# Kernel optimization log

Measured on AMD Instinct MI355X. Metric: run time of the kernel, lower is better.

The kernel has to match this reference:

```python
import jax, jax.numpy as jnp
import numpy as np

N, E, F, H, L = 100000, 800000, 128, 128, 64


def _glorot(key, shape):
    lim = float(np.sqrt(6.0 / (shape[0] + shape[1])))
    return jax.random.uniform(key, shape, jnp.float32, -lim, lim)


def setup_inputs() -> dict:
    key = jax.random.key(0)
    ks = jax.random.split(key, 10)
    x = jax.random.normal(ks[0], (N, F), jnp.float32)
    noise = jax.random.normal(ks[1], (N, F), jnp.float32)
    edge_index = jax.random.randint(ks[2], (2, E), 0, N, jnp.int32)
    return {
        "x": x,
        "noise": noise,
        "edge_index": edge_index,
        "bn_gamma": jnp.ones((F,), jnp.float32),
        "bn_beta": jnp.zeros((F,), jnp.float32),
        "W1": _glorot(ks[3], (F, H)),
        "b1": jnp.zeros((H,), jnp.float32),
        "W2": _glorot(ks[4], (H + 2 * F, H)),
        "b2": jnp.zeros((H,), jnp.float32),
        "Wm": _glorot(ks[5], (H + F, L)),
        "bm": jnp.zeros((L,), jnp.float32),
        "Ws": _glorot(ks[6], (H + F, L)),
        "bs": jnp.zeros((L,), jnp.float32),
    }


def _gcn_conv(x, W, b, src, dst, norm, n):
    # GCNConv: transform, then sym-normalized sparse aggregation, then bias
    h = x @ W                                 # [n, out]
    msg = h[src] * norm[:, None]              # gather + scale  [E', out]
    return jax.ops.segment_sum(msg, dst, num_segments=n) + b


def reference(x, noise, edge_index, bn_gamma, bn_beta, W1, b1, W2, b2, Wm, bm, Ws, bs):
    n = x.shape[0]
    loops = jnp.arange(n, dtype=edge_index.dtype)
    src = jnp.concatenate([edge_index[0], loops])  # add self-loops
    dst = jnp.concatenate([edge_index[1], loops])
    deg = jax.ops.segment_sum(jnp.ones_like(src, dtype=x.dtype), dst, num_segments=n)
    dinv = jnp.where(deg > 0, jax.lax.rsqrt(jnp.maximum(deg, 1e-12)), 0.0)
    norm = dinv[src] * dinv[dst]                   # D^-1/2 A D^-1/2 edge weights

    # bn1 (training-mode batch norm over nodes)
    mu = x.mean(axis=0)
    var = x.var(axis=0)
    xb = (x - mu) * jax.lax.rsqrt(var + 1e-5) * bn_gamma + bn_beta

    h1 = jax.nn.relu(_gcn_conv(xb, W1, b1, src, dst, norm, n))
    h1 = jnp.concatenate([xb, noise, h1], axis=1)  # [n, H + 2F]
    h2 = jax.nn.relu(_gcn_conv(h1, W2, b2, src, dst, norm, n))
    # dropout(p=0.4) in eval mode -> identity
    last = jnp.concatenate([xb, h2], axis=1)       # [n, F + H]
    z_mean = _gcn_conv(last, Wm, bm, src, dst, norm, n)
    z_logstd = _gcn_conv(last, Ws, bs, src, dst, norm, n)
    return (z_mean, z_logstd)
```

## Files before the change

### kernel.cpp

```cpp
#include <hip/hip_runtime.h>
#include <math.h>


typedef short bf16x8 __attribute__((ext_vector_type(8)));
typedef float f32x4 __attribute__((ext_vector_type(4)));
typedef float f32x2 __attribute__((ext_vector_type(2)));

#define BN_G 1024
#define SCAN_BLK 256
#define SCAN_ELEMS 1024

__device__ inline unsigned short f2bf(float f) {
    unsigned int u = __builtin_bit_cast(unsigned int, f);
    u += 0x7fff + ((u >> 16) & 1);
    return (unsigned short)(u >> 16);
}
__device__ inline float bfl(unsigned int u) { return __builtin_bit_cast(float, u << 16); }
__device__ inline float bfh(unsigned int u) { return __builtin_bit_cast(float, u & 0xffff0000u); }
__device__ inline unsigned int pack2(float lo, float hi) {
    return ((unsigned int)f2bf(hi) << 16) | f2bf(lo);
}
__device__ inline f32x2 unp(unsigned int u) {
    return (f32x2){__builtin_bit_cast(float, u << 16),
                   __builtin_bit_cast(float, u & 0xffff0000u)};
}
__device__ inline void acc8v(f32x2* a, uint4 v) {
    a[0] += unp(v.x); a[1] += unp(v.y); a[2] += unp(v.z); a[3] += unp(v.w);
}

__device__ __forceinline__ void gload_lds16(const void* g, void* l) {
    __builtin_amdgcn_global_load_lds(
        (const __attribute__((address_space(1))) unsigned int*)g,
        (__attribute__((address_space(3))) unsigned int*)l, 16, 0, 0);
}

__global__ __launch_bounds__(256) void fused1(const float4* __restrict__ x4,
                                              float* __restrict__ partials, int n,
                                              const int* __restrict__ ei,
                                              int* __restrict__ cnt,
                                              int* __restrict__ slot, int E) {
    __shared__ float4 lds[2][8][32];
    int bid = blockIdx.x, t = threadIdx.x;
    if (bid < BN_G) {
        int cg = t & 31;
        int rs = t >> 5;
        float4 s = make_float4(0.f, 0.f, 0.f, 0.f);
        float4 q = make_float4(0.f, 0.f, 0.f, 0.f);
        const float4 z4 = make_float4(0.f, 0.f, 0.f, 0.f);
        const int stride = BN_G * 32;
        for (int r0 = bid * 32 + rs * 4; r0 < n; r0 += stride) {
            float4 v0 = x4[(size_t)r0 * 32 + cg];
            float4 v1 = (r0 + 1 < n) ? x4[(size_t)(r0 + 1) * 32 + cg] : z4;
            float4 v2 = (r0 + 2 < n) ? x4[(size_t)(r0 + 2) * 32 + cg] : z4;
            float4 v3 = (r0 + 3 < n) ? x4[(size_t)(r0 + 3) * 32 + cg] : z4;
            s.x += v0.x + v1.x + v2.x + v3.x;
            s.y += v0.y + v1.y + v2.y + v3.y;
            s.z += v0.z + v1.z + v2.z + v3.z;
            s.w += v0.w + v1.w + v2.w + v3.w;
            q.x = fmaf(v0.x, v0.x, fmaf(v1.x, v1.x, fmaf(v2.x, v2.x, fmaf(v3.x, v3.x, q.x))));
            q.y = fmaf(v0.y, v0.y, fmaf(v1.y, v1.y, fmaf(v2.y, v2.y, fmaf(v3.y, v3.y, q.y))));
            q.z = fmaf(v0.z, v0.z, fmaf(v1.z, v1.z, fmaf(v2.z, v2.z, fmaf(v3.z, v3.z, q.z))));
            q.w = fmaf(v0.w, v0.w, fmaf(v1.w, v1.w, fmaf(v2.w, v2.w, fmaf(v3.w, v3.w, q.w))));
        }
        lds[0][rs][cg] = s;
        lds[1][rs][cg] = q;
        __syncthreads();
        if (t < 64) {
            int which = t >> 5;
            int c = t & 31;
            float4 a = lds[which][0][c];
#pragma unroll
            for (int i = 1; i < 8; i++) {
                float4 b = lds[which][i][c];
                a.x += b.x; a.y += b.y; a.z += b.z; a.w += b.w;
            }
            int base = which * 128 + c * 4;
            partials[(size_t)(base + 0) * BN_G + bid] = a.x;
            partials[(size_t)(base + 1) * BN_G + bid] = a.y;
            partials[(size_t)(base + 2) * BN_G + bid] = a.z;
            partials[(size_t)(base + 3) * BN_G + bid] = a.w;
        }
    } else {
        int e = (bid - BN_G) * 256 + t;
        if (e < E) slot[e] = atomicAdd(&cnt[ei[E + e]], 1);
    }
}

__global__ __launch_bounds__(256) void fused2(const float4* __restrict__ partials4,
                                              float* __restrict__ stats,
                                              const int* __restrict__ cnt,
                                              int* __restrict__ row_ptr,
                                              int* __restrict__ bsums, int n) {
    __shared__ float red[256];
    __shared__ int lds[SCAN_BLK];
    int t = threadIdx.x;
    if (blockIdx.x < 256) {
        int c = blockIdx.x;
        float4 v = partials4[(size_t)c * (BN_G / 4) + t];
        red[t] = v.x + v.y + v.z + v.w;
        __syncthreads();
        for (int off = 128; off > 0; off >>= 1) {
            if (t < off) red[t] += red[t + off];
            __syncthreads();
        }
        if (t == 0) stats[c] = red[0];
    } else {
        int blk = blockIdx.x - 256;
        int base = blk * SCAN_ELEMS;
        int v[4];
        int s = 0;
#pragma unroll
        for (int j = 0; j < 4; j++) {
            int i = base + t * 4 + j;
            v[j] = s;
            s += (i < n) ? cnt[i] : 0;
        }
        lds[t] = s;
        __syncthreads();
        for (int off = 1; off < SCAN_BLK; off <<= 1) {
            int val = (t >= off) ? lds[t - off] : 0;
            __syncthreads();
            lds[t] += val;
            __syncthreads();
        }
        int excl = (t == 0) ? 0 : lds[t - 1];
#pragma unroll
        for (int j = 0; j < 4; j++) {
            int i = base + t * 4 + j;
            if (i < n) row_ptr[i] = excl + v[j];
        }
        if (t == SCAN_BLK - 1) bsums[blk] = lds[t];
    }
}

__global__ void fused3(int* __restrict__ bsums, int nb,
                       const float* __restrict__ stats,
                       const float* __restrict__ gamma, const float* __restrict__ beta,
                       float* __restrict__ scale, float* __restrict__ shift, float invN) {
    int t = threadIdx.x;
    if (t == 0) {
        int acc = 0;
        for (int i = 0; i < nb; i++) { int c = bsums[i]; bsums[i] = acc; acc += c; }
    } else if (t >= 128 && t < 256) {
        int c = t - 128;
        float mu = stats[c] * invN;
        float var = stats[128 + c] * invN - mu * mu;
        float sc = gamma[c] / sqrtf(var + 1e-5f);
        scale[c] = sc;
        shift[c] = beta[c] - mu * sc;
    }
}

__global__ void fused4(int* __restrict__ row_ptr, const int* __restrict__ bsums,
                       const int* __restrict__ cnt, float* __restrict__ dinv,
                       int n, int E) {
    int i = blockIdx.x * blockDim.x + threadIdx.x;
    if (i < n) {
        row_ptr[i] += bsums[i / SCAN_ELEMS];
        dinv[i] = rsqrtf((float)cnt[i] + 1.0f);
    }
    if (i == 0) row_ptr[n] = E;
}

__device__ inline void pack_body(int i, const float* __restrict__ W,
                                 unsigned short* __restrict__ Wp,
                                 int K, int C, int colOff) {
    if (i >= K * C) return;
    int k = i / C, c = i % C;
    int gc = c + colOff;
    int s = k >> 7, kc = (k >> 5) & 3, lhi = (k >> 3) & 3, j = k & 7;
    int wc = gc >> 6, n = (gc >> 4) & 3, l15 = gc & 15;
    int lane = lhi * 16 + l15;
    size_t dst = ((size_t)((s * 2 + wc) * 4 + kc) * 4 + n) * 512 + lane * 8 + j;
    Wp[dst] = f2bf(W[i]);
}

__global__ __launch_bounds__(256) void fused5(
    const int* __restrict__ ei, const int* __restrict__ row_ptr,
    const int* __restrict__ slot, int* __restrict__ edge_src, int E, int EB,
    const float4* __restrict__ x4, const float4* __restrict__ n4,
    const float* __restrict__ scale, const float* __restrict__ shift,
    ushort4* __restrict__ xb, ushort4* __restrict__ nb4, int total4, int CB,
    const float* __restrict__ W1, unsigned short* __restrict__ Wp1,
    const float* __restrict__ W2, unsigned short* __restrict__ Wp2,
    const float* __restrict__ Wm, const float* __restrict__ Ws,
    unsigned short* __restrict__ Wpc)
{
    int bid = blockIdx.x, t = threadIdx.x;
    if (bid < EB) {
        int e = bid * 256 + t;
        if (e < E) {
            int s = ei[e], d = ei[E + e];
            edge_src[row_ptr[d] + slot[e]] = s;
        }
        return;
    }
    bid -= EB;
    if (bid < CB) {
        int i = bid * 256 + t;
        if (i < total4) {
            int c4 = (i & 31) << 2;
            float4 sc = *reinterpret_cast<const float4*>(scale + c4);
            float4 sh = *reinterpret_cast<const float4*>(shift + c4);
            float4 v = x4[i];
            ushort4 o;
            o.x = f2bf(fmaf(v.x, sc.x, sh.x));
            o.y = f2bf(fmaf(v.y, sc.y, sh.y));
            o.z = f2bf(fmaf(v.z, sc.z, sh.z));
            o.w = f2bf(fmaf(v.w, sc.w, sh.w));
            xb[i] = o;
            float4 w = n4[i];
            ushort4 p;
            p.x = f2bf(w.x); p.y = f2bf(w.y); p.z = f2bf(w.z); p.w = f2bf(w.w);
            nb4[i] = p;
        }
        return;
    }
    bid -= CB;
    if (bid < 64)  { pack_body(bid * 256 + t, W1, Wp1, 128, 128, 0); return; }
    bid -= 64;
    if (bid < 192) { pack_body(bid * 256 + t, W2, Wp2, 384, 128, 0); return; }
    bid -= 192;
    if (bid < 64)  { pack_body(bid * 256 + t, Wm, Wpc, 256, 64, 0); return; }
    bid -= 64;
    pack_body(bid * 256 + t, Ws, Wpc, 256, 64, 64);
}

template <int NSRC>
__global__ __launch_bounds__(256, 4) void gemm_mfma(
    const unsigned short* __restrict__ A0, const unsigned short* __restrict__ A1,
    const unsigned short* __restrict__ A2,
    const unsigned short* __restrict__ Wpk,
    const float* __restrict__ dinv, unsigned short* __restrict__ out)
{
    constexpr int NBUF = (NSRC > 1) ? 2 : 1;
    __shared__ unsigned char ldsA[NBUF][64 * 256];

    const int lane = threadIdx.x & 63;
    const int wid  = threadIdx.x >> 6;
    const int wr   = wid >> 1, wc = wid & 1;
    const int l15  = lane & 15, lhi = lane >> 4;
    const int c0   = wc * 64;
    const long rowblk = (long)blockIdx.x * 64;
    const int rl0 = wr * 32 + l15;
    const int rl1 = rl0 + 16;
    const int rsw = rl0 & 7;

    const unsigned short* __restrict__ srcs[3] = {A0, A1, A2};
    auto stage = [&](int s, int b) {
#pragma unroll
        for (int i = 0; i < 4; i++) {
            int G = (wid * 4 + i) * 64 + lane;
            int r = G >> 4, g = G & 15;
            const unsigned short* src = srcs[s] + (rowblk + r) * 128 + (g ^ (r & 7)) * 8;
            gload_lds16(src, &ldsA[b][G * 16]);
        }
    };

    f32x4 acc[2][4];
#pragma unroll
    for (int g = 0; g < 2; g++)
#pragma unroll
        for (int n = 0; n < 4; n++)
            acc[g][n] = (f32x4){0.f, 0.f, 0.f, 0.f};

    stage(0, 0);

#pragma unroll
    for (int s = 0; s < NSRC; s++) {
        const unsigned short* wbase = Wpk + ((size_t)(s * 2 + wc) * 16) * 512 + lane * 8;
        bf16x8 w[4][4];
#pragma unroll
        for (int kc = 0; kc < 4; kc++)
#pragma unroll
            for (int n = 0; n < 4; n++)
                w[kc][n] = *reinterpret_cast<const bf16x8*>(wbase + (kc * 4 + n) * 512);

        __syncthreads();
        if (s + 1 < NSRC) stage(s + 1, (s + 1) % NBUF);
        const unsigned char* bufp = ldsA[s % NBUF];

#pragma unroll
        for (int kc = 0; kc < 4; kc++) {
            int g0 = kc * 4 + lhi;
            bf16x8 a0 = *reinterpret_cast<const bf16x8*>(bufp + rl0 * 256 + (g0 ^ rsw) * 16);
            bf16x8 a1 = *reinterpret_cast<const bf16x8*>(bufp + rl1 * 256 + (g0 ^ rsw) * 16);
#pragma unroll
            for (int n = 0; n < 4; n++) {
                acc[0][n] = __builtin_amdgcn_mfma_f32_16x16x32_bf16(w[kc][n], a0, acc[0][n], 0, 0, 0);
                acc[1][n] = __builtin_amdgcn_mfma_f32_16x16x32_bf16(w[kc][n], a1, acc[1][n], 0, 0, 0);
            }
        }
    }

#pragma unroll
    for (int g = 0; g < 2; g++) {
        long row = rowblk + (g ? rl1 : rl0);
        float dv = dinv[row];
        unsigned short* op = out + row * 128 + c0 + lhi * 4;
#pragma unroll
        for (int n = 0; n < 4; n++) {
            f32x4 v = acc[g][n];
            ushort4 pk;
            pk.x = f2bf(v[0] * dv);
            pk.y = f2bf(v[1] * dv);
            pk.z = f2bf(v[2] * dv);
            pk.w = f2bf(v[3] * dv);
            *reinterpret_cast<ushort4*>(op + n * 16) = pk;
        }
    }
}

template <bool RELU>
__global__ void gather16(const uint4* __restrict__ hs4, const float* __restrict__ dinv,
                         const int* __restrict__ row_ptr, const int* __restrict__ edge_src,
                         const float* __restrict__ bias, uint4* __restrict__ out4, int n) {
    int node = blockIdx.x * 4 + (threadIdx.x >> 6);
    if (node >= n) return;
    int lane = threadIdx.x & 63;
    int cl = lane & 15, sub = lane >> 4;
    int beg = row_ptr[node], end = row_ptr[node + 1];
    f32x2 a0[4] = {(f32x2){0.f,0.f}, (f32x2){0.f,0.f}, (f32x2){0.f,0.f}, (f32x2){0.f,0.f}};
    f32x2 a1[4] = {(f32x2){0.f,0.f}, (f32x2){0.f,0.f}, (f32x2){0.f,0.f}, (f32x2){0.f,0.f}};
    if (sub == 0) acc8v(a0, hs4[(size_t)node * 16 + cl]);
    int e = beg + sub;
    for (; e + 4 < end; e += 8) {
        uint4 v0 = hs4[(size_t)edge_src[e] * 16 + cl];
        uint4 v1 = hs4[(size_t)edge_src[e + 4] * 16 + cl];
        acc8v(a0, v0);
        acc8v(a1, v1);
    }
    if (e < end) acc8v(a0, hs4[(size_t)edge_src[e] * 16 + cl]);
#pragma unroll
    for (int i = 0; i < 4; i++) a0[i] += a1[i];
#pragma unroll
    for (int i = 0; i < 4; i++) {
        a0[i].x += __shfl_xor(a0[i].x, 16);
        a0[i].y += __shfl_xor(a0[i].y, 16);
        a0[i].x += __shfl_xor(a0[i].x, 32);
        a0[i].y += __shfl_xor(a0[i].y, 32);
    }
    if (sub == 0) {
        float dv = dinv[node];
        float4 b0 = *reinterpret_cast<const float4*>(bias + cl * 8);
        float4 b1 = *reinterpret_cast<const float4*>(bias + cl * 8 + 4);
        float r0 = fmaf(a0[0].x, dv, b0.x), r1 = fmaf(a0[0].y, dv, b0.y);
        float r2 = fmaf(a0[1].x, dv, b0.z), r3 = fmaf(a0[1].y, dv, b0.w);
        float r4 = fmaf(a0[2].x, dv, b1.x), r5 = fmaf(a0[2].y, dv, b1.y);
        float r6 = fmaf(a0[3].x, dv, b1.z), r7 = fmaf(a0[3].y, dv, b1.w);
        if (RELU) {
            r0 = fmaxf(r0, 0.f); r1 = fmaxf(r1, 0.f); r2 = fmaxf(r2, 0.f); r3 = fmaxf(r3, 0.f);
            r4 = fmaxf(r4, 0.f); r5 = fmaxf(r5, 0.f); r6 = fmaxf(r6, 0.f); r7 = fmaxf(r7, 0.f);
        }
        uint4 o;
        o.x = pack2(r0, r1); o.y = pack2(r2, r3);
        o.z = pack2(r4, r5); o.w = pack2(r6, r7);
        out4[(size_t)node * 16 + cl] = o;
    }
}

__global__ void gather_dual(const uint4* __restrict__ hs4, const float* __restrict__ dinv,
                            const int* __restrict__ row_ptr, const int* __restrict__ edge_src,
                            const float* __restrict__ bm, const float* __restrict__ bs,
                            float* __restrict__ zm, float* __restrict__ zs, int n) {
    int node = blockIdx.x * 4 + (threadIdx.x >> 6);
    if (node >= n) return;
    int lane = threadIdx.x & 63;
    int cl = lane & 15, sub = lane >> 4;
    int beg = row_ptr[node], end = row_ptr[node + 1];
    f32x2 a0[4] = {(f32x2){0.f,0.f}, (f32x2){0.f,0.f}, (f32x2){0.f,0.f}, (f32x2){0.f,0.f}};
    f32x2 a1[4] = {(f32x2){0.f,0.f}, (f32x2){0.f,0.f}, (f32x2){0.f,0.f}, (f32x2){0.f,0.f}};
    if (sub == 0) acc8v(a0, hs4[(size_t)node * 16 + cl]);
    int e = beg + sub;
    for (; e + 4 < end; e += 8) {
        uint4 v0 = hs4[(size_t)edge_src[e] * 16 + cl];
        uint4 v1 = hs4[(size_t)edge_src[e + 4] * 16 + cl];
        acc8v(a0, v0);
        acc8v(a1, v1);
    }
    if (e < end) acc8v(a0, hs4[(size_t)edge_src[e] * 16 + cl]);
#pragma unroll
    for (int i = 0; i < 4; i++) a0[i] += a1[i];
#pragma unroll
    for (int i = 0; i < 4; i++) {
        a0[i].x += __shfl_xor(a0[i].x, 16);
        a0[i].y += __shfl_xor(a0[i].y, 16);
        a0[i].x += __shfl_xor(a0[i].x, 32);
        a0[i].y += __shfl_xor(a0[i].y, 32);
    }
    if (sub == 0) {
        float dv = dinv[node];
        const float* bp = (cl < 8) ? (bm + cl * 8) : (bs + (cl - 8) * 8);
        float* zp = (cl < 8) ? (zm + (size_t)node * 64 + cl * 8)
                             : (zs + (size_t)node * 64 + (cl - 8) * 8);
        float4 b0 = *reinterpret_cast<const float4*>(bp);
        float4 b1 = *reinterpret_cast<const float4*>(bp + 4);
        float4 o0 = make_float4(fmaf(a0[0].x, dv, b0.x), fmaf(a0[0].y, dv, b0.y),
                                fmaf(a0[1].x, dv, b0.z), fmaf(a0[1].y, dv, b0.w));
        float4 o1 = make_float4(fmaf(a0[2].x, dv, b1.x), fmaf(a0[2].y, dv, b1.y),
                                fmaf(a0[3].x, dv, b1.z), fmaf(a0[3].y, dv, b1.w));
        *reinterpret_cast<float4*>(zp) = o0;
        *reinterpret_cast<float4*>(zp + 4) = o1;
    }
}


extern "C" void kernel_launch(void* const* d_in, const int* in_sizes, int n_in,
                              void* d_out, int out_size, void* d_ws, size_t ws_size,
                              hipStream_t stream) {
    const float* x     = (const float*)d_in[0];
    const float* noise = (const float*)d_in[1];
    const int*   ei    = (const int*)d_in[2];
    const float* gamma = (const float*)d_in[3];
    const float* beta  = (const float*)d_in[4];
    const float* W1    = (const float*)d_in[5];
    const float* b1    = (const float*)d_in[6];
    const float* W2    = (const float*)d_in[7];
    const float* b2    = (const float*)d_in[8];
    const float* Wm    = (const float*)d_in[9];
    const float* bm    = (const float*)d_in[10];
    const float* Ws    = (const float*)d_in[11];
    const float* bs    = (const float*)d_in[12];

    const int N  = in_sizes[0] / 128;
    const int E  = in_sizes[2] / 2;
    const int NPAD = (N + 127) & ~127;
    const int nb = (N + SCAN_ELEMS - 1) / SCAN_ELEMS;
    const int EB = (E + 255) / 256;
    const int CB = (N * 32 + 255) / 256;

    auto align256 = [](size_t b) { return (b + 255) & ~(size_t)255; };
    char* p = (char*)d_ws;
    int* cnt      = (int*)p;  p += align256((size_t)N * 4);
    int* row_ptr  = (int*)p;  p += align256((size_t)(N + 1) * 4);
    int* edge_src = (int*)p;  p += align256((size_t)E * 4);
    int* slot     = (int*)p;  p += align256((size_t)E * 4);
    int* bsums    = (int*)p;  p += align256((size_t)nb * 4);
    float* dinv   = (float*)p; p += align256((size_t)NPAD * 4);
    float* stats  = (float*)p; p += align256(512 * 4);
    float* bnpart = (float*)p; p += align256((size_t)256 * BN_G * 4);
    unsigned short* Wp1 = (unsigned short*)p; p += align256(128 * 128 * 2);
    unsigned short* Wp2 = (unsigned short*)p; p += align256(128 * 384 * 2);
    unsigned short* Wpc = (unsigned short*)p; p += align256(128 * 256 * 2);
    unsigned short* xb16 = (unsigned short*)p; p += align256((size_t)NPAD * 128 * 2);
    unsigned short* n16  = (unsigned short*)p; p += align256((size_t)NPAD * 128 * 2);
    unsigned short* h16  = (unsigned short*)p; p += align256((size_t)NPAD * 128 * 2);

    float* scale = stats + 256;
    float* shift = stats + 384;

    float* dout = (float*)d_out;
    unsigned short* hs12 = (unsigned short*)d_out;
    unsigned short* hs3  = n16;
    float* zm = dout;
    float* zs = dout + (size_t)N * 64;

    const int gblocks = NPAD / 64;
    const int nblocks4 = (N + 3) / 4;

    hipMemsetAsync(cnt, 0, (size_t)N * 4, stream);
    fused1<<<BN_G + EB, 256, 0, stream>>>((const float4*)x, bnpart, N, ei, cnt, slot, E);
    fused2<<<256 + nb, 256, 0, stream>>>((const float4*)bnpart, stats, cnt, row_ptr, bsums, N);
    fused3<<<1, 256, 0, stream>>>(bsums, nb, stats, gamma, beta, scale, shift, 1.0f / (float)N);
    fused4<<<(N + 255) / 256, 256, 0, stream>>>(row_ptr, bsums, cnt, dinv, N, E);
    fused5<<<EB + CB + 384, 256, 0, stream>>>(
        ei, row_ptr, slot, edge_src, E, EB,
        (const float4*)x, (const float4*)noise, scale, shift,
        (ushort4*)xb16, (ushort4*)n16, N * 32, CB,
        W1, Wp1, W2, Wp2, Wm, Ws, Wpc);

    gemm_mfma<1><<<gblocks, 256, 0, stream>>>(xb16, nullptr, nullptr, Wp1, dinv, hs12);
    gather16<true><<<nblocks4, 256, 0, stream>>>((const uint4*)hs12, dinv, row_ptr,
                                                 edge_src, b1, (uint4*)h16, N);
    gemm_mfma<3><<<gblocks, 256, 0, stream>>>(xb16, n16, h16, Wp2, dinv, hs12);
    gather16<true><<<nblocks4, 256, 0, stream>>>((const uint4*)hs12, dinv, row_ptr,
                                                 edge_src, b2, (uint4*)h16, N);
    gemm_mfma<2><<<gblocks, 256, 0, stream>>>(xb16, h16, nullptr, Wpc, dinv, hs3);
    gather_dual<<<nblocks4, 256, 0, stream>>>((const uint4*)hs3, dinv, row_ptr,
                                              edge_src, bm, bs, zm, zs, N);
}
```

Before: 296.0 us.

## Fold fused3 into fused2 via last-block ticket and move noise cast earlier

Removes the single-block fused3 launch by having the last-finishing fused2 block (tracked with an atomic ticket) do the block-sum scan and BN scale/shift computation. The noise-to-bf16 conversion moves from fused5 into fused1 so it overlaps with the BN reduction and edge counting. Edge-count blocks now handle four edges per thread. This saves a kernel launch and shortens fused5, at the cost of an extra memset and a serialized tail in the last fused2 block.

After: 321.6 us. 1.09x slower.

```diff
diff --git a/kernel.cpp b/kernel.cpp
--- a/kernel.cpp
+++ b/kernel.cpp
@@ -15,8 +15,6 @@
     u += 0x7fff + ((u >> 16) & 1);
     return (unsigned short)(u >> 16);
 }
-__device__ inline float bfl(unsigned int u) { return __builtin_bit_cast(float, u << 16); }
-__device__ inline float bfh(unsigned int u) { return __builtin_bit_cast(float, u & 0xffff0000u); }
 __device__ inline unsigned int pack2(float lo, float hi) {
     return ((unsigned int)f2bf(hi) << 16) | f2bf(lo);
 }
@@ -38,7 +36,9 @@
                                               float* __restrict__ partials, int n,
                                               const int* __restrict__ ei,
                                               int* __restrict__ cnt,
-                                              int* __restrict__ slot, int E) {
+                                              int* __restrict__ slot, int E, int EB4,
+                                              const float4* __restrict__ n4,
+                                              ushort4* __restrict__ nb4, int total4) {
     __shared__ float4 lds[2][8][32];
     int bid = blockIdx.x, t = threadIdx.x;
     if (bid < BN_G) {
@@ -80,9 +80,25 @@
             partials[(size_t)(base + 2) * BN_G + bid] = a.z;
             partials[(size_t)(base + 3) * BN_G + bid] = a.w;
         }
-    } else {
-        int e = (bid - BN_G) * 256 + t;
-        if (e < E) slot[e] = atomicAdd(&cnt[ei[E + e]], 1);
+        return;
+    }
+    bid -= BN_G;
+    if (bid < EB4) {
+        int base = bid * 1024 + t;
+#pragma unroll
+        for (int i = 0; i < 4; i++) {
+            int e = base + i * 256;
+            if (e < E) slot[e] = atomicAdd(&cnt[ei[E + e]], 1);
+        }
+        return;
+    }
+    bid -= EB4;
+    int i = bid * 256 + t;
+    if (i < total4) {
+        float4 w = n4[i];
+        ushort4 p;
+        p.x = f2bf(w.x); p.y = f2bf(w.y); p.z = f2bf(w.z); p.w = f2bf(w.w);
+        nb4[i] = p;
     }
 }
 
@@ -90,9 +106,15 @@
                                               float* __restrict__ stats,
                                               const int* __restrict__ cnt,
                                               int* __restrict__ row_ptr,
-                                              int* __restrict__ bsums, int n) {
+                                              int* __restrict__ bsums, int n, int nb,
+                                              int* __restrict__ ticket,
+                                              const float* __restrict__ gamma,
+                                              const float* __restrict__ beta,
+                                              float* __restrict__ scale,
+                                              float* __restrict__ shift, float invN) {
     __shared__ float red[256];
     __shared__ int lds[SCAN_BLK];
+    __shared__ int amLast;
     int t = threadIdx.x;
     if (blockIdx.x < 256) {
         int c = blockIdx.x;
@@ -131,23 +153,24 @@
         }
         if (t == SCAN_BLK - 1) bsums[blk] = lds[t];
     }
-}
-
-__global__ void fused3(int* __restrict__ bsums, int nb,
-                       const float* __restrict__ stats,
-                       const float* __restrict__ gamma, const float* __restrict__ beta,
-                       float* __restrict__ scale, float* __restrict__ shift, float invN) {
-    int t = threadIdx.x;
-    if (t == 0) {
-        int acc = 0;
-        for (int i = 0; i < nb; i++) { int c = bsums[i]; bsums[i] = acc; acc += c; }
-    } else if (t >= 128 && t < 256) {
-        int c = t - 128;
-        float mu = stats[c] * invN;
-        float var = stats[128 + c] * invN - mu * mu;
-        float sc = gamma[c] / sqrtf(var + 1e-5f);
-        scale[c] = sc;
-        shift[c] = beta[c] - mu * sc;
+    __threadfence();
+    __syncthreads();
+    if (t == 0) amLast = (atomicAdd(ticket, 1) == 256 + nb - 1);
+    __syncthreads();
+    if (amLast) {
+        __threadfence();
+        if (t == 0) {
+            int acc = 0;
+            for (int i = 0; i < nb; i++) { int c = bsums[i]; bsums[i] = acc; acc += c; }
+        }
+        if (t >= 128 && t < 256) {
+            int c = t - 128;
+            float mu = stats[c] * invN;
+            float var = stats[128 + c] * invN - mu * mu;
+            float sc = gamma[c] / sqrtf(var + 1e-5f);
+            scale[c] = sc;
+            shift[c] = beta[c] - mu * sc;
+        }
     }
 }
 
@@ -178,9 +201,9 @@
 __global__ __launch_bounds__(256) void fused5(
     const int* __restrict__ ei, const int* __restrict__ row_ptr,
     const int* __restrict__ slot, int* __restrict__ edge_src, int E, int EB,
-    const float4* __restrict__ x4, const float4* __restrict__ n4,
+    const float4* __restrict__ x4,
     const float* __restrict__ scale, const float* __restrict__ shift,
-    ushort4* __restrict__ xb, ushort4* __restrict__ nb4, int total4, int CB,
+    ushort4* __restrict__ xb, int total4, int CB,
     const float* __restrict__ W1, unsigned short* __restrict__ Wp1,
     const float* __restrict__ W2, unsigned short* __restrict__ Wp2,
     const float* __restrict__ Wm, const float* __restrict__ Ws,
@@ -209,10 +232,6 @@
             o.z = f2bf(fmaf(v.z, sc.z, sh.z));
             o.w = f2bf(fmaf(v.w, sc.w, sh.w));
             xb[i] = o;
-            float4 w = n4[i];
-            ushort4 p;
-            p.x = f2bf(w.x); p.y = f2bf(w.y); p.z = f2bf(w.z); p.w = f2bf(w.w);
-            nb4[i] = p;
         }
         return;
     }
@@ -426,12 +445,14 @@
     const int E  = in_sizes[2] / 2;
     const int NPAD = (N + 127) & ~127;
     const int nb = (N + SCAN_ELEMS - 1) / SCAN_ELEMS;
-    const int EB = (E + 255) / 256;
-    const int CB = (N * 32 + 255) / 256;
+    const int EB  = (E + 255) / 256;
+    const int EB4 = (E + 1023) / 1024;
+    const int CB  = (N * 32 + 255) / 256;
 
     auto align256 = [](size_t b) { return (b + 255) & ~(size_t)255; };
     char* p = (char*)d_ws;
     int* cnt      = (int*)p;  p += align256((size_t)N * 4);
+    int* ticket   = (int*)p;  p += 256;
     int* row_ptr  = (int*)p;  p += align256((size_t)(N + 1) * 4);
     int* edge_src = (int*)p;  p += align256((size_t)E * 4);
     int* slot     = (int*)p;  p += align256((size_t)E * 4);
@@ -459,14 +480,17 @@
     const int nblocks4 = (N + 3) / 4;
 
     hipMemsetAsync(cnt, 0, (size_t)N * 4, stream);
-    fused1<<<BN_G + EB, 256, 0, stream>>>((const float4*)x, bnpart, N, ei, cnt, slot, E);
-    fused2<<<256 + nb, 256, 0, stream>>>((const float4*)bnpart, stats, cnt, row_ptr, bsums, N);
-    fused3<<<1, 256, 0, stream>>>(bsums, nb, stats, gamma, beta, scale, shift, 1.0f / (float)N);
+    hipMemsetAsync(ticket, 0, 4, stream);
+    fused1<<<BN_G + EB4 + CB, 256, 0, stream>>>(
+        (const float4*)x, bnpart, N, ei, cnt, slot, E, EB4,
+        (const float4*)noise, (ushort4*)n16, N * 32);
+    fused2<<<256 + nb, 256, 0, stream>>>((const float4*)bnpart, stats, cnt, row_ptr,
+                                         bsums, N, nb, ticket, gamma, beta,
+                                         scale, shift, 1.0f / (float)N);
     fused4<<<(N + 255) / 256, 256, 0, stream>>>(row_ptr, bsums, cnt, dinv, N, E);
     fused5<<<EB + CB + 384, 256, 0, stream>>>(
         ei, row_ptr, slot, edge_src, E, EB,
-        (const float4*)x, (const float4*)noise, scale, shift,
-        (ushort4*)xb16, (ushort4*)n16, N * 32, CB,
+        (const float4*)x, scale, shift, (ushort4*)xb16, N * 32, CB,
         W1, Wp1, W2, Wp2, Wm, Ws, Wpc);
 
     gemm_mfma<1><<<gblocks, 256, 0, stream>>>(xb16, nullptr, nullptr, Wp1, dinv, hs12);
```
